# Optimization experiments

Measured on AMD Instinct MI355X. Metric: run time of the kernel, lower is better.

## Reference

```python
import jax, jax.numpy as jnp
import numpy as np

EPS = 1e-5

def conv2d(x, w, b=None, pad=1):
    # x: [B,C,H,W], w: [O,I,kh,kw]
    y = jax.lax.conv_general_dilated(x, w, (1, 1), [(pad, pad), (pad, pad)],
                                     dimension_numbers=('NCHW', 'OIHW', 'NCHW'))
    if b is not None:
        y = y + b[None, :, None, None]
    return y

def bn(x, g, b, m, v):
    # inference-mode batchnorm
    inv = g / jnp.sqrt(v + EPS)
    return x * inv[None, :, None, None] + (b - m * inv)[None, :, None, None]

def coord_conv(x, w, b):
    B, C, H, W = x.shape
    yy = jnp.broadcast_to(jnp.linspace(-1.0, 1.0, H)[:, None], (H, W))
    xx = jnp.broadcast_to(jnp.linspace(-1.0, 1.0, W)[None, :], (H, W))
    coords = jnp.broadcast_to(jnp.stack([xx, yy])[None], (B, 2, H, W)).astype(x.dtype)
    return conv2d(jnp.concatenate([x, coords], axis=1), w, b, pad=1)

def deform_conv(x, offset, w):
    # deformable conv v1, 3x3, pad=1, stride=1, no bias
    B, C, H, W = x.shape
    K = 9
    # offset channels interleaved (y, x) per kernel tap
    off = offset.reshape(B, K, 2, H, W)
    off_y, off_x = off[:, :, 0], off[:, :, 1]          # [B,9,H,W]
    k = jnp.arange(K)
    ko_y = (k // 3 - 1).astype(x.dtype)[None, :, None, None]
    ko_x = (k % 3 - 1).astype(x.dtype)[None, :, None, None]
    base_y = jnp.arange(H, dtype=x.dtype)[None, None, :, None]
    base_x = jnp.arange(W, dtype=x.dtype)[None, None, None, :]
    py = base_y + ko_y + off_y                          # [B,9,H,W]
    px = base_x + ko_x + off_x
    xf = x.reshape(B, C, H * W)
    y0 = jnp.floor(py)
    x0 = jnp.floor(px)
    acc = jnp.zeros((B, C, K, H, W), x.dtype)
    for dy in (0.0, 1.0):
        for dx in (0.0, 1.0):
            yy = y0 + dy
            xx = x0 + dx
            wgt = (1.0 - jnp.abs(py - yy)) * (1.0 - jnp.abs(px - xx))
            valid = (yy >= 0) & (yy < H) & (xx >= 0) & (xx < W)
            wgt = jnp.where(valid, wgt, 0.0)            # zero padding OOB
            yi = jnp.clip(yy, 0, H - 1).astype(jnp.int32)
            xi = jnp.clip(xx, 0, W - 1).astype(jnp.int32)
            idx = (yi * W + xi).reshape(B, K * H * W)
            v = jnp.take_along_axis(xf, idx[:, None, :], axis=2).reshape(B, C, K, H, W)
            acc = acc + v * wgt[:, None]
    wk = w.reshape(w.shape[0], w.shape[1], K)           # [O,I,9]
    return jnp.einsum('bckhw,ock->bohw', acc, wk)

def setup_inputs() -> dict:
    key = jax.random.key(0)
    ks = jax.random.split(key, 16)
    d_model, hd = 256, 64
    B, H, W = 8, 96, 96
    f32 = jnp.float32
    def bn_params(k):
        k1, k2, k3 = jax.random.split(k, 3)
        return (1.0 + 0.1 * jax.random.normal(k1, (hd,), f32),
                0.1 * jax.random.normal(k2, (hd,), f32),
                0.1 * jax.random.normal(k3, (hd,), f32),
                0.5 + jax.random.uniform(jax.random.fold_in(k, 7), (hd,), f32))
    bn1 = bn_params(ks[1]); bn2 = bn_params(ks[2]); bn3 = bn_params(ks[3]); bn4 = bn_params(ks[4])
    inp = {
        'features': jax.random.normal(ks[0], (B, H, W, d_model), f32),
        'coord_w': 0.05 * jax.random.normal(ks[5], (hd, d_model + 2, 3, 3), f32),
        'coord_b': jnp.zeros((hd,), f32),
        'bn1_g': bn1[0], 'bn1_b': bn1[1], 'bn1_m': bn1[2], 'bn1_v': bn1[3],
        'off_w': 0.01 * jax.random.normal(ks[6], (18, hd, 3, 3), f32),
        'off_b': 0.01 * jax.random.normal(ks[7], (18,), f32),
        'dc_w': 0.05 * jax.random.normal(ks[8], (hd, hd, 3, 3), f32),
        'bn2_g': bn2[0], 'bn2_b': bn2[1], 'bn2_m': bn2[2], 'bn2_v': bn2[3],
        'r1_w': 0.05 * jax.random.normal(ks[9], (hd, hd, 3, 3), f32),
        'bn3_g': bn3[0], 'bn3_b': bn3[1], 'bn3_m': bn3[2], 'bn3_v': bn3[3],
        'r2_w': 0.05 * jax.random.normal(ks[10], (hd, hd, 3, 3), f32),
        'bn4_g': bn4[0], 'bn4_b': bn4[1], 'bn4_m': bn4[2], 'bn4_v': bn4[3],
        'out_w': 0.1 * jax.random.normal(ks[11], (1, hd, 1, 1), f32),
        'out_b': jnp.zeros((1,), f32),
    }
    return inp

def reference(features, coord_w, coord_b, bn1_g, bn1_b, bn1_m, bn1_v,
              off_w, off_b, dc_w, bn2_g, bn2_b, bn2_m, bn2_v,
              r1_w, bn3_g, bn3_b, bn3_m, bn3_v,
              r2_w, bn4_g, bn4_b, bn4_m, bn4_v, out_w, out_b):
    x = jnp.transpose(features, (0, 3, 1, 2))           # NHWC -> NCHW
    x = jax.nn.relu(bn(coord_conv(x, coord_w, coord_b), bn1_g, bn1_b, bn1_m, bn1_v))
    offset = conv2d(x, off_w, off_b, pad=1)
    x = deform_conv(x, offset, dc_w)
    x = jax.nn.relu(bn(x, bn2_g, bn2_b, bn2_m, bn2_v))
    x = jax.nn.relu(bn(conv2d(x, r1_w, None, pad=1), bn3_g, bn3_b, bn3_m, bn3_v))
    x = jax.nn.relu(bn(conv2d(x, r2_w, None, pad=1), bn4_g, bn4_b, bn4_m, bn4_v))
    return jax.nn.sigmoid(conv2d(x, out_w, out_b, pad=0))
```

## Files before the change

kernel.cpp:

```cpp
#include <hip/hip_runtime.h>


typedef unsigned short u16;
typedef unsigned int u32;
typedef __attribute__((ext_vector_type(8)))  short bf16x8;
typedef __attribute__((ext_vector_type(16))) float f32x16;

#define EPSBN 1e-5f

__device__ __forceinline__ u16 f2bf(float f) {
  u32 u = __builtin_bit_cast(u32, f);
  u32 r = u + 0x7FFFu + ((u >> 16) & 1u);
  return (u16)(r >> 16);
}
__device__ __forceinline__ u32 pk2(float a, float b) {
  return (u32)f2bf(a) | ((u32)f2bf(b) << 16);
}
__device__ __forceinline__ float lo2f(u32 w) { return __builtin_bit_cast(float, w << 16); }
__device__ __forceinline__ float hi2f(u32 w) { return __builtin_bit_cast(float, w & 0xFFFF0000u); }

#define N_WCF 147456
#define N_WCC 9216
#define N_WOF 18432
#define N_W64 36864
#define N_ALLW (N_WCF + N_WCC + N_WOF + 3*N_W64)

__global__ __launch_bounds__(256) void prep_kernel(
    const float* __restrict__ coord_w, const float* __restrict__ off_w,
    const float* __restrict__ dc_w, const float* __restrict__ r1_w,
    const float* __restrict__ r2_w,
    u16* __restrict__ wcf, u16* __restrict__ wcc, u16* __restrict__ wof,
    u16* __restrict__ wdf, u16* __restrict__ wr1, u16* __restrict__ wr2)
{
  int i = blockIdx.x * 256 + threadIdx.x;
  if (i >= N_ALLW) return;
  int d = i;
  if (d < N_WCF) {
    int j = d & 7, lane = (d >> 3) & 63, frag = d >> 9;
    int nt = frag & 1, h = (frag >> 1) & 3, tap = (frag >> 3) % 9, cc = (frag >> 3) / 9;
    int ic = cc * 64 + h * 16 + ((lane >> 5) << 3) + j;
    int oc = nt * 32 + (lane & 31);
    wcf[d] = f2bf(coord_w[((size_t)oc * 258 + ic) * 9 + tap]);
    return;
  }
  d -= N_WCF;
  if (d < N_WCC) {
    int j = d & 7, lane = (d >> 3) & 63, frag = d >> 9;
    int nt = frag & 1, tap = frag >> 1;
    int ic = 256 + ((lane >> 5) << 3) + j;
    int oc = nt * 32 + (lane & 31);
    wcc[d] = (ic < 258) ? f2bf(coord_w[((size_t)oc * 258 + ic) * 9 + tap]) : (u16)0;
    return;
  }
  d -= N_WCC;
  if (d < N_WOF) {
    int j = d & 7, lane = (d >> 3) & 63, frag = d >> 9;
    int h = frag & 3, tap = frag >> 2;
    int ic = h * 16 + ((lane >> 5) << 3) + j;
    int oc = lane & 31;
    wof[d] = (oc < 18) ? f2bf(off_w[((size_t)oc * 64 + ic) * 9 + tap]) : (u16)0;
    return;
  }
  d -= N_WOF;
  int seg = d / N_W64;
  int e = d - seg * N_W64;
  int j = e & 7, lane = (e >> 3) & 63, frag = e >> 9;
  int nt = frag & 1, h = (frag >> 1) & 3, tap = frag >> 3;
  int ic = h * 16 + ((lane >> 5) << 3) + j;
  int oc = nt * 32 + (lane & 31);
  const float* src = (seg == 0) ? dc_w : (seg == 1) ? r1_w : r2_w;
  u16* dst = (seg == 0) ? wdf : (seg == 1) ? wr1 : wr2;
  dst[e] = f2bf(src[((size_t)oc * 64 + ic) * 9 + tap]);
}

__global__ __launch_bounds__(256, 4) void coord_conv_kernel(
    const float* __restrict__ feat, const u16* __restrict__ wcf,
    const u16* __restrict__ wcc, const float* __restrict__ cb,
    const float* __restrict__ g, const float* __restrict__ bb,
    const float* __restrict__ m, const float* __restrict__ v,
    u16* __restrict__ x1b)
{
  __shared__ __align__(16) u16 tile[6 * 34 * 72];
  const int t = threadIdx.x;
  const int wv = t >> 6, lane = t & 63;
  const int l31 = lane & 31, l5 = lane >> 5;
  const int x0 = blockIdx.x * 32, y0 = blockIdx.y * 4, b = blockIdx.z;

  f32x16 acc[2] = {};

  for (int cc = 0; cc < 4; ++cc) {
    __syncthreads();
    for (int i = t; i < 1632; i += 256) {
      const int px = i >> 3, gg = i & 7;
      const int ly = px / 34, lx = px - ly * 34;
      const int gy = y0 + ly - 1, gx = x0 + lx - 1;
      uint4 o = {0u, 0u, 0u, 0u};
      if ((unsigned)gy < 96u && (unsigned)gx < 96u) {
        const float* p = feat + ((size_t)((b * 96 + gy) * 96 + gx)) * 256
                         + cc * 64 + gg * 8;
        const float4 f0 = *(const float4*)p;
        const float4 f1 = *(const float4*)(p + 4);
        o.x = pk2(f0.x, f0.y); o.y = pk2(f0.z, f0.w);
        o.z = pk2(f1.x, f1.y); o.w = pk2(f1.z, f1.w);
      }
      *(uint4*)(tile + (ly * 34 + lx) * 72 + gg * 8) = o;
    }
    __syncthreads();
    #pragma unroll
    for (int tap = 0; tap < 9; ++tap) {
      const int dy = tap / 3, dx = tap - dy * 3;
      #pragma unroll
      for (int h = 0; h < 4; ++h) {
        const bf16x8 afr = *(const bf16x8*)(tile +
            ((wv + dy) * 34 + l31 + dx) * 72 + h * 16 + l5 * 8);
        #pragma unroll
        for (int nt = 0; nt < 2; ++nt) {
          const bf16x8 bfr = *(const bf16x8*)(wcf +
              ((size_t)((((cc * 9 + tap) * 4 + h) * 2) + nt)) * 512 + lane * 8);
          acc[nt] = __builtin_amdgcn_mfma_f32_32x32x16_bf16(afr, bfr, acc[nt],
                                                            0, 0, 0);
        }
      }
    }
  }

  __syncthreads();
  for (int i = t; i < 408; i += 256) {
    const int px = i >> 1, gg = i & 1;
    const int ly = px / 34, lx = px - ly * 34;
    const int gy = y0 + ly - 1, gx = x0 + lx - 1;
    uint4 o = {0u, 0u, 0u, 0u};
    if (gg == 0 && (unsigned)gy < 96u && (unsigned)gx < 96u) {
      const float xx = -1.f + (2.f / 95.f) * (float)gx;
      const float yy = -1.f + (2.f / 95.f) * (float)gy;
      o.x = pk2(xx, yy);
    }
    *(uint4*)(tile + (ly * 34 + lx) * 72 + gg * 8) = o;
  }
  __syncthreads();
  #pragma unroll
  for (int tap = 0; tap < 9; ++tap) {
    const int dy = tap / 3, dx = tap - dy * 3;
    const bf16x8 afr = *(const bf16x8*)(tile +
        ((wv + dy) * 34 + l31 + dx) * 72 + l5 * 8);
    #pragma unroll
    for (int nt = 0; nt < 2; ++nt) {
      const bf16x8 bfr = *(const bf16x8*)(wcc +
          ((size_t)(tap * 2 + nt)) * 512 + lane * 8);
      acc[nt] = __builtin_amdgcn_mfma_f32_32x32x16_bf16(afr, bfr, acc[nt],
                                                        0, 0, 0);
    }
  }

  const int y = y0 + wv;
  #pragma unroll
  for (int nt = 0; nt < 2; ++nt) {
    const int oc = nt * 32 + l31;
    const float inv = g[oc] * rsqrtf(v[oc] + EPSBN);
    const float sh = bb[oc] - m[oc] * inv + cb[oc] * inv;
    #pragma unroll
    for (int r = 0; r < 16; ++r) {
      const int xr = (r & 3) + 8 * (r >> 2) + 4 * l5;
      const float val = fmaxf(fmaf(acc[nt][r], inv, sh), 0.f);
      x1b[((size_t)((b * 96 + y) * 96 + x0 + xr)) * 64 + oc] = f2bf(val);
    }
  }
}

template<int NN, int EPI>
__global__ __launch_bounds__(256, 4) void conv64_kernel(
    const u16* __restrict__ xin, const u16* __restrict__ wf,
    const float* __restrict__ bias,
    const float* __restrict__ g, const float* __restrict__ bb,
    const float* __restrict__ m, const float* __restrict__ v,
    const float* __restrict__ ow, const float* __restrict__ ob,
    void* __restrict__ outp)
{
  __shared__ __align__(16) u16 tile[6 * 34 * 72];
  __shared__ float red[128];
  const int t = threadIdx.x;
  const int wv = t >> 6, lane = t & 63;
  const int l31 = lane & 31, l5 = lane >> 5;
  const int x0 = blockIdx.x * 32, y0 = blockIdx.y * 4, b = blockIdx.z;

  for (int i = t; i < 1632; i += 256) {
    const int px = i >> 3, gg = i & 7;
    const int ly = px / 34, lx = px - ly * 34;
    const int gy = y0 + ly - 1, gx = x0 + lx - 1;
    uint4 o = {0u, 0u, 0u, 0u};
    if ((unsigned)gy < 96u && (unsigned)gx < 96u)
      o = *(const uint4*)(xin + (((size_t)((b * 96 + gy) * 96 + gx)) << 6)
                          + gg * 8);
    *(uint4*)(tile + (ly * 34 + lx) * 72 + gg * 8) = o;
  }
  __syncthreads();

  f32x16 acc[NN] = {};
  #pragma unroll
  for (int tap = 0; tap < 9; ++tap) {
    const int dy = tap / 3, dx = tap - dy * 3;
    #pragma unroll
    for (int h = 0; h < 4; ++h) {
      const bf16x8 afr = *(const bf16x8*)(tile +
          ((wv + dy) * 34 + l31 + dx) * 72 + h * 16 + l5 * 8);
      #pragma unroll
      for (int nt = 0; nt < NN; ++nt) {
        const bf16x8 bfr = *(const bf16x8*)(wf +
            ((size_t)((tap * 4 + h) * NN + nt)) * 512 + lane * 8);
        acc[nt] = __builtin_amdgcn_mfma_f32_32x32x16_bf16(afr, bfr, acc[nt],
                                                          0, 0, 0);
      }
    }
  }

  const int y = y0 + wv;
  if constexpr (EPI == 0) {
    u16* xo = (u16*)outp;
    #pragma unroll
    for (int nt = 0; nt < NN; ++nt) {
      const int oc = nt * 32 + l31;
      const float inv = g[oc] * rsqrtf(v[oc] + EPSBN);
      const float sh = bb[oc] - m[oc] * inv;
      #pragma unroll
      for (int r = 0; r < 16; ++r) {
        const int xr = (r & 3) + 8 * (r >> 2) + 4 * l5;
        const float val = fmaxf(fmaf(acc[nt][r], inv, sh), 0.f);
        xo[((size_t)((b * 96 + y) * 96 + x0 + xr)) * 64 + oc] = f2bf(val);
      }
    }
  } else if constexpr (EPI == 1) {
    float* fo = (float*)outp;
    const int oc = l31;
    if (oc < 18) {
      const float bs = bias[oc];
      #pragma unroll
      for (int r = 0; r < 16; ++r) {
        const int xr = (r & 3) + 8 * (r >> 2) + 4 * l5;
        fo[((size_t)((b * 96 + y) * 96 + x0 + xr)) * 18 + oc] = acc[0][r] + bs;
      }
    }
  } else {
    float pr[16];
    #pragma unroll
    for (int r = 0; r < 16; ++r) pr[r] = 0.f;
    #pragma unroll
    for (int nt = 0; nt < NN; ++nt) {
      const int oc = nt * 32 + l31;
      const float inv = g[oc] * rsqrtf(v[oc] + EPSBN);
      const float sh = bb[oc] - m[oc] * inv;
      const float wo = ow[oc];
      #pragma unroll
      for (int r = 0; r < 16; ++r) {
        const float val = fmaxf(fmaf(acc[nt][r], inv, sh), 0.f);
        pr[r] = fmaf(val, wo, pr[r]);
      }
    }
    #pragma unroll
    for (int mask = 1; mask <= 16; mask <<= 1)
      #pragma unroll
      for (int r = 0; r < 16; ++r)
        pr[r] += __shfl_xor(pr[r], mask);
    if (l31 == 0) {
      #pragma unroll
      for (int r = 0; r < 16; ++r) {
        const int xr = (r & 3) + 8 * (r >> 2) + 4 * l5;
        red[wv * 32 + xr] = pr[r];
      }
    }
    __syncthreads();
    if (t < 128) {
      float* fo = (float*)outp;
      const int yy = y0 + (t >> 5), xx = x0 + (t & 31);
      const float val = red[t] + ob[0];
      fo[(size_t)(b * 96 + yy) * 96 + xx] = 1.f / (1.f + expf(-val));
    }
  }
}

__global__ __launch_bounds__(256, 4) void deform_kernel(
    const u16* __restrict__ x1b, const float* __restrict__ off,
    const u16* __restrict__ wdf,
    const float* __restrict__ g, const float* __restrict__ bb,
    const float* __restrict__ m, const float* __restrict__ v,
    u16* __restrict__ x2b)
{
  __shared__ __align__(16) u16 s[128 * 72];
  __shared__ float offs[128 * 18];
  const int t = threadIdx.x;
  const int wv = t >> 6, lane = t & 63;
  const int l31 = lane & 31, l5 = lane >> 5;
  const int x0 = blockIdx.x * 16, y0 = blockIdx.y * 8, b = blockIdx.z;

  for (int i = t; i < 2304; i += 256) {
    const int p = i / 18, c = i - p * 18;
    const int gy = y0 + (p >> 4), gx = x0 + (p & 15);
    offs[i] = off[((size_t)((b * 96 + gy) * 96 + gx)) * 18 + c];
  }

  f32x16 acc[2] = {};

  for (int k = 0; k < 9; ++k) {
    __syncthreads();
    #pragma unroll
    for (int rr = 0; rr < 2; ++rr) {
      const int role = t + rr * 256;
      const int sp = role >> 2, part = role & 3;
      const int sy = y0 + (sp >> 4), sx = x0 + (sp & 15);
      const float oy = offs[sp * 18 + 2 * k];
      const float ox = offs[sp * 18 + 2 * k + 1];
      const float py = (float)(sy + k / 3 - 1) + oy;
      const float px = (float)(sx + k % 3 - 1) + ox;
      const float yf = floorf(py), xf = floorf(px);
      const float fy = py - yf, fx = px - xf;
      const int yi = (int)yf, xi = (int)xf;
      float val[16];
      #pragma unroll
      for (int j = 0; j < 16; ++j) val[j] = 0.f;
      #pragma unroll
      for (int cor = 0; cor < 4; ++cor) {
        const int cy = yi + (cor >> 1), cx = xi + (cor & 1);
        if ((unsigned)cy < 96u && (unsigned)cx < 96u) {
          const float wy = (cor & 2) ? fy : 1.f - fy;
          const float wx = (cor & 1) ? fx : 1.f - fx;
          const float wgt = wy * wx;
          const u16* sp2 = x1b + ((size_t)((b * 96 + cy) * 96 + cx)) * 64
                           + part * 16;
          const uint4 ua = *(const uint4*)sp2;
          const uint4 ub = *(const uint4*)(sp2 + 8);
          const u32 uu[8] = {ua.x, ua.y, ua.z, ua.w, ub.x, ub.y, ub.z, ub.w};
          #pragma unroll
          for (int u = 0; u < 8; ++u) {
            val[2 * u]     = fmaf(wgt, lo2f(uu[u]), val[2 * u]);
            val[2 * u + 1] = fmaf(wgt, hi2f(uu[u]), val[2 * u + 1]);
          }
        }
      }
      u32 pk[8];
      #pragma unroll
      for (int u = 0; u < 8; ++u) pk[u] = pk2(val[2 * u], val[2 * u + 1]);
      uint4 w0 = {pk[0], pk[1], pk[2], pk[3]};
      uint4 w1 = {pk[4], pk[5], pk[6], pk[7]};
      *(uint4*)(s + sp * 72 + part * 16) = w0;
      *(uint4*)(s + sp * 72 + part * 16 + 8) = w1;
    }
    __syncthreads();
    #pragma unroll
    for (int h = 0; h < 4; ++h) {
      const bf16x8 afr = *(const bf16x8*)(s + (wv * 32 + l31) * 72
                                          + h * 16 + l5 * 8);
      #pragma unroll
      for (int nt = 0; nt < 2; ++nt) {
        const bf16x8 bfr = *(const bf16x8*)(wdf +
            ((size_t)((k * 4 + h) * 2 + nt)) * 512 + lane * 8);
        acc[nt] = __builtin_amdgcn_mfma_f32_32x32x16_bf16(afr, bfr, acc[nt],
                                                          0, 0, 0);
      }
    }
  }

  #pragma unroll
  for (int nt = 0; nt < 2; ++nt) {
    const int oc = nt * 32 + l31;
    const float inv = g[oc] * rsqrtf(v[oc] + EPSBN);
    const float sh = bb[oc] - m[oc] * inv;
    #pragma unroll
    for (int r = 0; r < 16; ++r) {
      const int pxi = wv * 32 + (r & 3) + 8 * (r >> 2) + 4 * l5;
      const int y = y0 + (pxi >> 4), x = x0 + (pxi & 15);
      const float val = fmaxf(fmaf(acc[nt][r], inv, sh), 0.f);
      x2b[((size_t)((b * 96 + y) * 96 + x)) * 64 + oc] = f2bf(val);
    }
  }
}

extern "C" void kernel_launch(void* const* d_in, const int* in_sizes, int n_in,
                              void* d_out, int out_size, void* d_ws,
                              size_t ws_size, hipStream_t stream)
{
  (void)in_sizes; (void)n_in; (void)out_size; (void)ws_size;
  const float* features = (const float*)d_in[0];
  const float* coord_w  = (const float*)d_in[1];
  const float* coord_b  = (const float*)d_in[2];
  const float* bn1g = (const float*)d_in[3];
  const float* bn1b = (const float*)d_in[4];
  const float* bn1m = (const float*)d_in[5];
  const float* bn1v = (const float*)d_in[6];
  const float* off_w = (const float*)d_in[7];
  const float* off_b = (const float*)d_in[8];
  const float* dc_w  = (const float*)d_in[9];
  const float* bn2g = (const float*)d_in[10];
  const float* bn2b = (const float*)d_in[11];
  const float* bn2m = (const float*)d_in[12];
  const float* bn2v = (const float*)d_in[13];
  const float* r1_w = (const float*)d_in[14];
  const float* bn3g = (const float*)d_in[15];
  const float* bn3b = (const float*)d_in[16];
  const float* bn3m = (const float*)d_in[17];
  const float* bn3v = (const float*)d_in[18];
  const float* r2_w = (const float*)d_in[19];
  const float* bn4g = (const float*)d_in[20];
  const float* bn4b = (const float*)d_in[21];
  const float* bn4m = (const float*)d_in[22];
  const float* bn4v = (const float*)d_in[23];
  const float* out_w = (const float*)d_in[24];
  const float* out_b = (const float*)d_in[25];

  char* W = (char*)d_ws;
  float* offb = (float*)W;
  u16*   x1b  = (u16*)(W + 5308416);
  u16*   x2b  = (u16*)(W + 14745600);
  u16*   x3b  = (u16*)(W + 24182784);
  u16*   wcf  = (u16*)(W + 33619968);
  u16*   wcc  = wcf + N_WCF;
  u16*   wof  = wcc + N_WCC;
  u16*   wdf  = wof + N_WOF;
  u16*   wr1  = wdf + N_W64;
  u16*   wr2  = wr1 + N_W64;

  prep_kernel<<<(N_ALLW + 255) / 256, 256, 0, stream>>>(
      coord_w, off_w, dc_w, r1_w, r2_w, wcf, wcc, wof, wdf, wr1, wr2);

  dim3 grid(3, 24, 8);
  dim3 gridD(6, 12, 8);

  coord_conv_kernel<<<grid, 256, 0, stream>>>(
      features, wcf, wcc, coord_b, bn1g, bn1b, bn1m, bn1v, x1b);
  conv64_kernel<1, 1><<<grid, 256, 0, stream>>>(
      x1b, wof, off_b, nullptr, nullptr, nullptr, nullptr, nullptr, nullptr,
      (void*)offb);
  deform_kernel<<<gridD, 256, 0, stream>>>(
      x1b, offb, wdf, bn2g, bn2b, bn2m, bn2v, x2b);
  conv64_kernel<2, 0><<<grid, 256, 0, stream>>>(
      x2b, wr1, nullptr, bn3g, bn3b, bn3m, bn3v, nullptr, nullptr, (void*)x3b);
  conv64_kernel<2, 2><<<grid, 256, 0, stream>>>(
      x3b, wr2, nullptr, bn4g, bn4b, bn4m, bn4v, out_w, out_b, d_out);
}
```

Before: 270.7 us.

## Prefetch next input-channel chunk into registers during MFMA in coord conv

In the coord conv kernel, global loads for the next 64-channel chunk are issued into registers before the MFMA loop over the current chunk, and packed into shared memory on the next iteration. This double-buffers through registers so load latency overlaps with compute, at the cost of more registers, which is why launch bounds drop from 4 to 3 blocks. The conv64 and deform kernels also unroll their tile and offset loads so all global loads issue before any shared-memory stores.

Result: faster. 259.7 us (-4.1%).

```diff
diff --git a/kernel.cpp b/kernel.cpp
--- a/kernel.cpp
+++ b/kernel.cpp
@@ -73,7 +73,7 @@
   dst[e] = f2bf(src[((size_t)oc * 64 + ic) * 9 + tap]);
 }
 
-__global__ __launch_bounds__(256, 4) void coord_conv_kernel(
+__global__ __launch_bounds__(256, 3) void coord_conv_kernel(
     const float* __restrict__ feat, const u16* __restrict__ wcf,
     const u16* __restrict__ wcc, const float* __restrict__ cb,
     const float* __restrict__ g, const float* __restrict__ bb,
@@ -87,25 +87,47 @@
   const int x0 = blockIdx.x * 32, y0 = blockIdx.y * 4, b = blockIdx.z;
 
   f32x16 acc[2] = {};
-
+  float4 pa[7], pb[7];
+
+  auto issue = [&](int cc) {
+    #pragma unroll
+    for (int r = 0; r < 7; ++r) {
+      const int i = t + r * 256;
+      const float4 z = {0.f, 0.f, 0.f, 0.f};
+      pa[r] = z; pb[r] = z;
+      if (i < 1632) {
+        const int px = i >> 3, gg = i & 7;
+        const int ly = px / 34, lx = px - ly * 34;
+        const int gy = y0 + ly - 1, gx = x0 + lx - 1;
+        if ((unsigned)gy < 96u && (unsigned)gx < 96u) {
+          const float* p = feat + ((size_t)((b * 96 + gy) * 96 + gx)) * 256
+                           + cc * 64 + gg * 8;
+          pa[r] = *(const float4*)p;
+          pb[r] = *(const float4*)(p + 4);
+        }
+      }
+    }
+  };
+  auto commit = [&]() {
+    #pragma unroll
+    for (int r = 0; r < 7; ++r) {
+      const int i = t + r * 256;
+      if (i < 1632) {
+        const int px = i >> 3, gg = i & 7;
+        uint4 o;
+        o.x = pk2(pa[r].x, pa[r].y); o.y = pk2(pa[r].z, pa[r].w);
+        o.z = pk2(pb[r].x, pb[r].y); o.w = pk2(pb[r].z, pb[r].w);
+        *(uint4*)(tile + px * 72 + gg * 8) = o;
+      }
+    }
+  };
+
+  issue(0);
   for (int cc = 0; cc < 4; ++cc) {
     __syncthreads();
-    for (int i = t; i < 1632; i += 256) {
-      const int px = i >> 3, gg = i & 7;
-      const int ly = px / 34, lx = px - ly * 34;
-      const int gy = y0 + ly - 1, gx = x0 + lx - 1;
-      uint4 o = {0u, 0u, 0u, 0u};
-      if ((unsigned)gy < 96u && (unsigned)gx < 96u) {
-        const float* p = feat + ((size_t)((b * 96 + gy) * 96 + gx)) * 256
-                         + cc * 64 + gg * 8;
-        const float4 f0 = *(const float4*)p;
-        const float4 f1 = *(const float4*)(p + 4);
-        o.x = pk2(f0.x, f0.y); o.y = pk2(f0.z, f0.w);
-        o.z = pk2(f1.x, f1.y); o.w = pk2(f1.z, f1.w);
-      }
-      *(uint4*)(tile + (ly * 34 + lx) * 72 + gg * 8) = o;
-    }
+    commit();
     __syncthreads();
+    if (cc < 3) issue(cc + 1);
     #pragma unroll
     for (int tap = 0; tap < 9; ++tap) {
       const int dy = tap / 3, dx = tap - dy * 3;
@@ -183,15 +205,28 @@
   const int l31 = lane & 31, l5 = lane >> 5;
   const int x0 = blockIdx.x * 32, y0 = blockIdx.y * 4, b = blockIdx.z;
 
-  for (int i = t; i < 1632; i += 256) {
-    const int px = i >> 3, gg = i & 7;
-    const int ly = px / 34, lx = px - ly * 34;
-    const int gy = y0 + ly - 1, gx = x0 + lx - 1;
-    uint4 o = {0u, 0u, 0u, 0u};
-    if ((unsigned)gy < 96u && (unsigned)gx < 96u)
-      o = *(const uint4*)(xin + (((size_t)((b * 96 + gy) * 96 + gx)) << 6)
-                          + gg * 8);
-    *(uint4*)(tile + (ly * 34 + lx) * 72 + gg * 8) = o;
+  uint4 pf[7];
+  #pragma unroll
+  for (int r = 0; r < 7; ++r) {
+    const int i = t + r * 256;
+    const uint4 z = {0u, 0u, 0u, 0u};
+    pf[r] = z;
+    if (i < 1632) {
+      const int px = i >> 3, gg = i & 7;
+      const int ly = px / 34, lx = px - ly * 34;
+      const int gy = y0 + ly - 1, gx = x0 + lx - 1;
+      if ((unsigned)gy < 96u && (unsigned)gx < 96u)
+        pf[r] = *(const uint4*)(xin + (((size_t)((b * 96 + gy) * 96 + gx)) << 6)
+                                + gg * 8);
+    }
+  }
+  #pragma unroll
+  for (int r = 0; r < 7; ++r) {
+    const int i = t + r * 256;
+    if (i < 1632) {
+      const int px = i >> 3, gg = i & 7;
+      *(uint4*)(tile + px * 72 + gg * 8) = pf[r];
+    }
   }
   __syncthreads();
 
@@ -291,10 +326,17 @@
   const int l31 = lane & 31, l5 = lane >> 5;
   const int x0 = blockIdx.x * 16, y0 = blockIdx.y * 8, b = blockIdx.z;
 
-  for (int i = t; i < 2304; i += 256) {
-    const int p = i / 18, c = i - p * 18;
-    const int gy = y0 + (p >> 4), gx = x0 + (p & 15);
-    offs[i] = off[((size_t)((b * 96 + gy) * 96 + gx)) * 18 + c];
+  {
+    float po[9];
+    #pragma unroll
+    for (int r = 0; r < 9; ++r) {
+      const int i = t + r * 256;
+      const int p = i / 18, c = i - p * 18;
+      const int gy = y0 + (p >> 4), gx = x0 + (p & 15);
+      po[r] = off[((size_t)((b * 96 + gy) * 96 + gx)) * 18 + c];
+    }
+    #pragma unroll
+    for (int r = 0; r < 9; ++r) offs[t + r * 256] = po[r];
   }
 
   f32x16 acc[2] = {};
```
